# Optimization experiments

Hardware: AMD Instinct MI355X
Metric: run time of the kernel (lower is better)

The kernel has to match this reference:

```python
import jax, jax.numpy as jnp
import numpy as np

Q, S, D = 8192, 30, 512
THRESH = 30


def setup_inputs() -> dict:
    key = jax.random.key(0)
    ks = jax.random.split(key, 8)
    return {
        "query_encode": jax.random.normal(ks[0], (Q, D), jnp.float32),
        "support_encode": jax.random.normal(ks[1], (S, D), jnp.float32),
        # binary CTR-style labels in {0,1}
        "support_y": jnp.round(jax.random.uniform(ks[2], (1, S), jnp.float32)),
        "support_predict": jax.random.normal(ks[3], (S,), jnp.float32),
        "query_predict": jax.random.normal(ks[4], (Q,), jnp.float32),
        "fc1_w": jax.random.normal(ks[5], (D,), jnp.float32) / np.sqrt(D),
        "fc1_b": jnp.zeros((), jnp.float32),
        # AdjustLayer params: scale init 6, bias init 0, shape [THRESH, 1]
        "adjust_scale": jnp.full((THRESH, 1), 6.0, jnp.float32),
        "adjust_bias": jnp.zeros((THRESH, 1), jnp.float32),
        "num_samples": S,
    }


def reference(query_encode, support_encode, support_y, support_predict,
              query_predict, fc1_w, fc1_b, adjust_scale, adjust_bias,
              num_samples):
    # Pairwise L1 distance: [Q, S, D]
    distance = jnp.abs(query_encode[:, None, :] - support_encode[None, :, :])
    # Linear scorer over feature dim -> [Q, S]
    similar_score = jnp.einsum("qsd,d->qs", distance, fc1_w) + fc1_b
    attn = jax.nn.softmax(similar_score, axis=1)  # softmax over support dim
    # Residual of support labels vs predictor output: [1, S]
    delta_y = support_y - jax.nn.sigmoid(support_predict)[None, :]
    delta_y_hat = jnp.sum(delta_y * attn, axis=1)  # [Q]
    # AdjustLayer: indexed scale/bias (index is a static int here)
    scale = jnp.abs(adjust_scale[num_samples - 1, 0])
    bias = adjust_bias[num_samples - 1, 0]
    prediction = delta_y_hat * scale + bias + query_predict  # [Q]
    # Mean L2 distance to support set: [Q]
    mean_l2 = jnp.mean(jnp.sqrt(jnp.sum(distance ** 2, axis=-1)), axis=-1)
    return prediction, mean_l2
```

## Files before the change

kernel.cpp:

```cpp
#include <hip/hip_runtime.h>
#include <math.h>


#define QN 8192
#define SN 30
#define DN 512
#define QPB 16
#define BLK 512
#define RS 516

__global__ __launch_bounds__(BLK, 2)
void resus_one(const float* __restrict__ query,
               const float* __restrict__ support,
               const float* __restrict__ support_y,
               const float* __restrict__ support_pr,
               const float* __restrict__ query_pr,
               const float* __restrict__ fc1_w,
               const float* __restrict__ adj_scale,
               const float* __restrict__ adj_bias,
               const int*   __restrict__ num_samples,
               float* __restrict__ out)
{
    __shared__ float s_lds[SN * RS];

    const int tid = threadIdx.x;

    {
        const float4* sg = reinterpret_cast<const float4*>(support);
        for (int i = tid; i < SN * (DN / 4); i += BLK) {
            const int row = i >> 7;
            const int c4  = i & 127;
            *reinterpret_cast<float4*>(s_lds + row * RS + 4 * c4) = sg[i];
        }
    }
    __syncthreads();

    const int lane = tid & 63;
    const int wv   = tid >> 6;
    const int h    = lane >> 5;
    const int s    = lane & 31;
    const int srow_i = (s < SN) ? s : (SN - 1);

    const int q0 = blockIdx.x * QPB + wv * 2;
    const int q1 = q0 + 1;

    const float* srow = s_lds + srow_i * RS + h * 256;
    const float* qr0  = query + (size_t)q0 * DN + h * 256;
    const float* qr1  = query + (size_t)q1 * DN + h * 256;
    const float* wr   = fc1_w + h * 256;

    float sc0 = 0.f, sq0 = 0.f, sc1 = 0.f, sq1 = 0.f;

#define ACC4(QV, SV, WV, SC, SQ) { \
    float d0_ = (QV).x - (SV).x; SC = fmaf((WV).x, fabsf(d0_), SC); SQ = fmaf(d0_, d0_, SQ); \
    float d1_ = (QV).y - (SV).y; SC = fmaf((WV).y, fabsf(d1_), SC); SQ = fmaf(d1_, d1_, SQ); \
    float d2_ = (QV).z - (SV).z; SC = fmaf((WV).z, fabsf(d2_), SC); SQ = fmaf(d2_, d2_, SQ); \
    float d3_ = (QV).w - (SV).w; SC = fmaf((WV).w, fabsf(d3_), SC); SQ = fmaf(d3_, d3_, SQ); }

#pragma unroll 4
    for (int j = 0; j < 32; ++j) {
        const float4 sa = *reinterpret_cast<const float4*>(srow + 8 * j);
        const float4 sb = *reinterpret_cast<const float4*>(srow + 8 * j + 4);
        const float4 wa = *reinterpret_cast<const float4*>(wr + 8 * j);
        const float4 wb = *reinterpret_cast<const float4*>(wr + 8 * j + 4);
        const float4 a0 = *reinterpret_cast<const float4*>(qr0 + 8 * j);
        const float4 b0 = *reinterpret_cast<const float4*>(qr0 + 8 * j + 4);
        const float4 a1 = *reinterpret_cast<const float4*>(qr1 + 8 * j);
        const float4 b1 = *reinterpret_cast<const float4*>(qr1 + 8 * j + 4);
        ACC4(a0, sa, wa, sc0, sq0)
        ACC4(b0, sb, wb, sc0, sq0)
        ACC4(a1, sa, wa, sc1, sq1)
        ACC4(b1, sb, wb, sc1, sq1)
    }
#undef ACC4

    sc0 += __shfl_xor(sc0, 32);
    sq0 += __shfl_xor(sq0, 32);
    sc1 += __shfl_xor(sc1, 32);
    sq1 += __shfl_xor(sq1, 32);

    const bool valid = (s < SN);
    float scv = h ? sc1 : sc0;
    float ssv = h ? sq1 : sq0;
    const int q = h ? q1 : q0;

    float dy = 0.f;
    if (valid)
        dy = support_y[s] - 1.0f / (1.0f + expf(-support_pr[s]));
    if (!valid) { scv = -1e30f; ssv = 0.f; }

    float m = scv;
#pragma unroll
    for (int off = 16; off >= 1; off >>= 1)
        m = fmaxf(m, __shfl_xor(m, off));

    float e   = valid ? expf(scv - m) : 0.f;
    float den = e;
    float num = dy * e;
    float l2  = valid ? sqrtf(ssv) : 0.f;
#pragma unroll
    for (int off = 16; off >= 1; off >>= 1) {
        den += __shfl_xor(den, off);
        num += __shfl_xor(num, off);
        l2  += __shfl_xor(l2, off);
    }

    if (s == 0) {
        const int ns = num_samples[0];
        const float scale = fabsf(adj_scale[ns - 1]);
        const float bias  = adj_bias[ns - 1];
        out[q]      = num / den * scale + bias + query_pr[q];
        out[QN + q] = l2 * (1.0f / (float)SN);
    }
}

extern "C" void kernel_launch(void* const* d_in, const int* in_sizes, int n_in,
                              void* d_out, int out_size, void* d_ws, size_t ws_size,
                              hipStream_t stream)
{
    const float* query      = (const float*)d_in[0];
    const float* support    = (const float*)d_in[1];
    const float* support_y  = (const float*)d_in[2];
    const float* support_pr = (const float*)d_in[3];
    const float* query_pr   = (const float*)d_in[4];
    const float* fc1_w      = (const float*)d_in[5];
    const float* adj_scale  = (const float*)d_in[7];
    const float* adj_bias   = (const float*)d_in[8];
    const int*   num_s      = (const int*)d_in[9];
    float* out = (float*)d_out;

    dim3 grid(QN / QPB);
    hipLaunchKernelGGL(resus_one, grid, dim3(BLK), 0, stream,
                       query, support, support_y, support_pr, query_pr,
                       fc1_w, adj_scale, adj_bias, num_s, out);
}
```

Before: 105.2 us.

## Process four queries per wave with prefetched query loads and odd LDS stride

```diff
diff --git a/kernel.cpp b/kernel.cpp
--- a/kernel.cpp
+++ b/kernel.cpp
@@ -5,9 +5,11 @@
 #define QN 8192
 #define SN 30
 #define DN 512
-#define QPB 16
 #define BLK 512
-#define RS 516
+#define WPB 8
+#define QPW 4
+#define QPB (WPB * QPW)
+#define RS 515
 
 __global__ __launch_bounds__(BLK, 2)
 void resus_one(const float* __restrict__ query,
@@ -23,95 +25,128 @@
 {
     __shared__ float s_lds[SN * RS];
 
-    const int tid = threadIdx.x;
-
-    {
-        const float4* sg = reinterpret_cast<const float4*>(support);
-        for (int i = tid; i < SN * (DN / 4); i += BLK) {
-            const int row = i >> 7;
-            const int c4  = i & 127;
-            *reinterpret_cast<float4*>(s_lds + row * RS + 4 * c4) = sg[i];
-        }
-    }
-    __syncthreads();
-
+    const int tid  = threadIdx.x;
     const int lane = tid & 63;
     const int wv   = tid >> 6;
     const int h    = lane >> 5;
     const int s    = lane & 31;
     const int srow_i = (s < SN) ? s : (SN - 1);
 
-    const int q0 = blockIdx.x * QPB + wv * 2;
-    const int q1 = q0 + 1;
+    const int qbase = blockIdx.x * QPB + wv * QPW;
 
+    const float* qr0 = query + (size_t)(qbase + 0) * DN + h * 256;
+    const float* qr1 = query + (size_t)(qbase + 1) * DN + h * 256;
+    const float* qr2 = query + (size_t)(qbase + 2) * DN + h * 256;
+    const float* qr3 = query + (size_t)(qbase + 3) * DN + h * 256;
+    const float* wr  = fc1_w + h * 256;
     const float* srow = s_lds + srow_i * RS + h * 256;
-    const float* qr0  = query + (size_t)q0 * DN + h * 256;
-    const float* qr1  = query + (size_t)q1 * DN + h * 256;
-    const float* wr   = fc1_w + h * 256;
+
+    float4 c0a = *reinterpret_cast<const float4*>(qr0);
+    float4 c0b = *reinterpret_cast<const float4*>(qr0 + 4);
+    float4 c1a = *reinterpret_cast<const float4*>(qr1);
+    float4 c1b = *reinterpret_cast<const float4*>(qr1 + 4);
+    float4 c2a = *reinterpret_cast<const float4*>(qr2);
+    float4 c2b = *reinterpret_cast<const float4*>(qr2 + 4);
+    float4 c3a = *reinterpret_cast<const float4*>(qr3);
+    float4 c3b = *reinterpret_cast<const float4*>(qr3 + 4);
+    float4 cwa = *reinterpret_cast<const float4*>(wr);
+    float4 cwb = *reinterpret_cast<const float4*>(wr + 4);
+
+    {
+        const float4* sg = reinterpret_cast<const float4*>(support);
+        for (int i = tid; i < SN * (DN / 4); i += BLK) {
+            const float4 v = sg[i];
+            float* d = s_lds + (i >> 7) * RS + 4 * (i & 127);
+            d[0] = v.x; d[1] = v.y; d[2] = v.z; d[3] = v.w;
+        }
+    }
+    __syncthreads();
 
     float sc0 = 0.f, sq0 = 0.f, sc1 = 0.f, sq1 = 0.f;
+    float sc2 = 0.f, sq2 = 0.f, sc3 = 0.f, sq3 = 0.f;
 
-#define ACC4(QV, SV, WV, SC, SQ) { \
-    float d0_ = (QV).x - (SV).x; SC = fmaf((WV).x, fabsf(d0_), SC); SQ = fmaf(d0_, d0_, SQ); \
-    float d1_ = (QV).y - (SV).y; SC = fmaf((WV).y, fabsf(d1_), SC); SQ = fmaf(d1_, d1_, SQ); \
-    float d2_ = (QV).z - (SV).z; SC = fmaf((WV).z, fabsf(d2_), SC); SQ = fmaf(d2_, d2_, SQ); \
-    float d3_ = (QV).w - (SV).w; SC = fmaf((WV).w, fabsf(d3_), SC); SQ = fmaf(d3_, d3_, SQ); }
+#define ACC8(CA, CB, SC, SQ) { float d_; \
+    d_ = (CA).x - s0; SC = fmaf(cwa.x, fabsf(d_), SC); SQ = fmaf(d_, d_, SQ); \
+    d_ = (CA).y - s1; SC = fmaf(cwa.y, fabsf(d_), SC); SQ = fmaf(d_, d_, SQ); \
+    d_ = (CA).z - s2; SC = fmaf(cwa.z, fabsf(d_), SC); SQ = fmaf(d_, d_, SQ); \
+    d_ = (CA).w - s3; SC = fmaf(cwa.w, fabsf(d_), SC); SQ = fmaf(d_, d_, SQ); \
+    d_ = (CB).x - s4; SC = fmaf(cwb.x, fabsf(d_), SC); SQ = fmaf(d_, d_, SQ); \
+    d_ = (CB).y - s5; SC = fmaf(cwb.y, fabsf(d_), SC); SQ = fmaf(d_, d_, SQ); \
+    d_ = (CB).z - s6; SC = fmaf(cwb.z, fabsf(d_), SC); SQ = fmaf(d_, d_, SQ); \
+    d_ = (CB).w - s7; SC = fmaf(cwb.w, fabsf(d_), SC); SQ = fmaf(d_, d_, SQ); }
 
 #pragma unroll 4
     for (int j = 0; j < 32; ++j) {
-        const float4 sa = *reinterpret_cast<const float4*>(srow + 8 * j);
-        const float4 sb = *reinterpret_cast<const float4*>(srow + 8 * j + 4);
-        const float4 wa = *reinterpret_cast<const float4*>(wr + 8 * j);
-        const float4 wb = *reinterpret_cast<const float4*>(wr + 8 * j + 4);
-        const float4 a0 = *reinterpret_cast<const float4*>(qr0 + 8 * j);
-        const float4 b0 = *reinterpret_cast<const float4*>(qr0 + 8 * j + 4);
-        const float4 a1 = *reinterpret_cast<const float4*>(qr1 + 8 * j);
-        const float4 b1 = *reinterpret_cast<const float4*>(qr1 + 8 * j + 4);
-        ACC4(a0, sa, wa, sc0, sq0)
-        ACC4(b0, sb, wb, sc0, sq0)
-        ACC4(a1, sa, wa, sc1, sq1)
-        ACC4(b1, sb, wb, sc1, sq1)
+        const int jn = (j + 1) & 31;
+        float4 n0a = *reinterpret_cast<const float4*>(qr0 + 8 * jn);
+        float4 n0b = *reinterpret_cast<const float4*>(qr0 + 8 * jn + 4);
+        float4 n1a = *reinterpret_cast<const float4*>(qr1 + 8 * jn);
+        float4 n1b = *reinterpret_cast<const float4*>(qr1 + 8 * jn + 4);
+        float4 n2a = *reinterpret_cast<const float4*>(qr2 + 8 * jn);
+        float4 n2b = *reinterpret_cast<const float4*>(qr2 + 8 * jn + 4);
+        float4 n3a = *reinterpret_cast<const float4*>(qr3 + 8 * jn);
+        float4 n3b = *reinterpret_cast<const float4*>(qr3 + 8 * jn + 4);
+        float4 nwa = *reinterpret_cast<const float4*>(wr + 8 * jn);
+        float4 nwb = *reinterpret_cast<const float4*>(wr + 8 * jn + 4);
+
+        const float* sp = srow + 8 * j;
+        const float s0 = sp[0], s1 = sp[1], s2 = sp[2], s3 = sp[3];
+        const float s4 = sp[4], s5 = sp[5], s6 = sp[6], s7 = sp[7];
+
+        ACC8(c0a, c0b, sc0, sq0)
+        ACC8(c1a, c1b, sc1, sq1)
+        ACC8(c2a, c2b, sc2, sq2)
+        ACC8(c3a, c3b, sc3, sq3)
+
+        c0a = n0a; c0b = n0b; c1a = n1a; c1b = n1b;
+        c2a = n2a; c2b = n2b; c3a = n3a; c3b = n3b;
+        cwa = nwa; cwb = nwb;
     }
-#undef ACC4
+#undef ACC8
 
-    sc0 += __shfl_xor(sc0, 32);
-    sq0 += __shfl_xor(sq0, 32);
-    sc1 += __shfl_xor(sc1, 32);
-    sq1 += __shfl_xor(sq1, 32);
+    sc0 += __shfl_xor(sc0, 32); sq0 += __shfl_xor(sq0, 32);
+    sc1 += __shfl_xor(sc1, 32); sq1 += __shfl_xor(sq1, 32);
+    sc2 += __shfl_xor(sc2, 32); sq2 += __shfl_xor(sq2, 32);
+    sc3 += __shfl_xor(sc3, 32); sq3 += __shfl_xor(sq3, 32);
 
     const bool valid = (s < SN);
-    float scv = h ? sc1 : sc0;
-    float ssv = h ? sq1 : sq0;
-    const int q = h ? q1 : q0;
-
     float dy = 0.f;
     if (valid)
         dy = support_y[s] - 1.0f / (1.0f + expf(-support_pr[s]));
-    if (!valid) { scv = -1e30f; ssv = 0.f; }
 
-    float m = scv;
-#pragma unroll
-    for (int off = 16; off >= 1; off >>= 1)
-        m = fmaxf(m, __shfl_xor(m, off));
+    const int ns = num_samples[0];
+    const float ascale = fabsf(adj_scale[ns - 1]);
+    const float abias  = adj_bias[ns - 1];
 
-    float e   = valid ? expf(scv - m) : 0.f;
-    float den = e;
-    float num = dy * e;
-    float l2  = valid ? sqrtf(ssv) : 0.f;
-#pragma unroll
-    for (int off = 16; off >= 1; off >>= 1) {
-        den += __shfl_xor(den, off);
-        num += __shfl_xor(num, off);
-        l2  += __shfl_xor(l2, off);
-    }
+    float scA = h ? sc2 : sc0;  float sqA = h ? sq2 : sq0;
+    float scB = h ? sc3 : sc1;  float sqB = h ? sq3 : sq1;
+    const int qA = qbase + 2 * h;
+    const int qB = qA + 1;
 
-    if (s == 0) {
-        const int ns = num_samples[0];
-        const float scale = fabsf(adj_scale[ns - 1]);
-        const float bias  = adj_bias[ns - 1];
-        out[q]      = num / den * scale + bias + query_pr[q];
-        out[QN + q] = l2 * (1.0f / (float)SN);
-    }
+#define FINISH(SCV, SQV, QI) { \
+    float scv = (SCV), ssv = (SQV); \
+    if (!valid) { scv = -1e30f; ssv = 0.f; } \
+    float m_ = scv; \
+    _Pragma("unroll") \
+    for (int off = 16; off >= 1; off >>= 1) m_ = fmaxf(m_, __shfl_xor(m_, off)); \
+    float e_   = valid ? expf(scv - m_) : 0.f; \
+    float den_ = e_; \
+    float num_ = dy * e_; \
+    float l2_  = valid ? sqrtf(ssv) : 0.f; \
+    _Pragma("unroll") \
+    for (int off = 16; off >= 1; off >>= 1) { \
+        den_ += __shfl_xor(den_, off); \
+        num_ += __shfl_xor(num_, off); \
+        l2_  += __shfl_xor(l2_,  off); \
+    } \
+    if (s == 0) { \
+        out[(QI)]      = num_ / den_ * ascale + abias + query_pr[(QI)]; \
+        out[QN + (QI)] = l2_ * (1.0f / (float)SN); \
+    } }
+
+    FINISH(scA, sqA, qA)
+    FINISH(scB, sqB, qB)
+#undef FINISH
 }
 
 extern "C" void kernel_launch(void* const* d_in, const int* in_sizes, int n_in,
```

Measured after the change: 104.5 us. No clear change (-0.7%).

## Keep query slices in registers and stream support rows through LDS with atomic partials

Applied to the files above, without the earlier changes.

```diff
diff --git a/kernel.cpp b/kernel.cpp
--- a/kernel.cpp
+++ b/kernel.cpp
@@ -5,9 +5,10 @@
 #define QN 8192
 #define SN 30
 #define DN 512
-#define QPB 16
-#define BLK 512
-#define RS 516
+#define BLK 256
+#define QT 16
+#define SROW 572
+#define SCHUNK 15
 
 __global__ __launch_bounds__(BLK, 2)
 void resus_one(const float* __restrict__ query,
@@ -21,96 +22,125 @@
                const int*   __restrict__ num_samples,
                float* __restrict__ out)
 {
-    __shared__ float s_lds[SN * RS];
+    __shared__ float  sp[SCHUNK * SROW];
+    __shared__ float2 part[QT * SN];
 
-    const int tid = threadIdx.x;
+    const int tid  = threadIdx.x;
+    const int ql   = tid & 15;
+    const int dseg = tid >> 4;
+    const int q    = blockIdx.x * QT + ql;
 
     {
-        const float4* sg = reinterpret_cast<const float4*>(support);
-        for (int i = tid; i < SN * (DN / 4); i += BLK) {
-            const int row = i >> 7;
-            const int c4  = i & 127;
-            *reinterpret_cast<float4*>(s_lds + row * RS + 4 * c4) = sg[i];
+        float* pf = reinterpret_cast<float*>(part);
+        for (int i = tid; i < QT * SN * 2; i += BLK) pf[i] = 0.0f;
+    }
+
+    const float* qp = query + (size_t)q * DN + dseg * 32;
+    const float4 q0 = *reinterpret_cast<const float4*>(qp +  0);
+    const float4 q1 = *reinterpret_cast<const float4*>(qp +  4);
+    const float4 q2 = *reinterpret_cast<const float4*>(qp +  8);
+    const float4 q3 = *reinterpret_cast<const float4*>(qp + 12);
+    const float4 q4 = *reinterpret_cast<const float4*>(qp + 16);
+    const float4 q5 = *reinterpret_cast<const float4*>(qp + 20);
+    const float4 q6 = *reinterpret_cast<const float4*>(qp + 24);
+    const float4 q7 = *reinterpret_cast<const float4*>(qp + 28);
+    const float* wp = fc1_w + dseg * 32;
+    const float4 w0 = *reinterpret_cast<const float4*>(wp +  0);
+    const float4 w1 = *reinterpret_cast<const float4*>(wp +  4);
+    const float4 w2 = *reinterpret_cast<const float4*>(wp +  8);
+    const float4 w3 = *reinterpret_cast<const float4*>(wp + 12);
+    const float4 w4 = *reinterpret_cast<const float4*>(wp + 16);
+    const float4 w5 = *reinterpret_cast<const float4*>(wp + 20);
+    const float4 w6 = *reinterpret_cast<const float4*>(wp + 24);
+    const float4 w7 = *reinterpret_cast<const float4*>(wp + 28);
+
+    const int sbase = dseg * 36;
+
+#define ACC4(QV, WV, SV) { float d_; \
+    d_ = (QV).x - (SV).x; sc = fmaf((WV).x, fabsf(d_), sc); sq = fmaf(d_, d_, sq); \
+    d_ = (QV).y - (SV).y; sc = fmaf((WV).y, fabsf(d_), sc); sq = fmaf(d_, d_, sq); \
+    d_ = (QV).z - (SV).z; sc = fmaf((WV).z, fabsf(d_), sc); sq = fmaf(d_, d_, sq); \
+    d_ = (QV).w - (SV).w; sc = fmaf((WV).w, fabsf(d_), sc); sq = fmaf(d_, d_, sq); }
+
+    for (int pass = 0; pass < 2; ++pass) {
+        __syncthreads();
+
+        const float4* sg = reinterpret_cast<const float4*>(
+            support + (size_t)pass * SCHUNK * DN);
+        for (int i = tid; i < SCHUNK * 128; i += BLK) {
+            const int row = i >> 7, c4 = i & 127;
+            *reinterpret_cast<float4*>(
+                sp + row * SROW + 36 * (c4 >> 3) + 4 * (c4 & 7)) = sg[i];
+        }
+        __syncthreads();
+
+#pragma unroll 3
+        for (int sl = 0; sl < SCHUNK; ++sl) {
+            const float* sr = sp + sl * SROW + sbase;
+            const float4 s0 = *reinterpret_cast<const float4*>(sr +  0);
+            const float4 s1 = *reinterpret_cast<const float4*>(sr +  4);
+            const float4 s2 = *reinterpret_cast<const float4*>(sr +  8);
+            const float4 s3 = *reinterpret_cast<const float4*>(sr + 12);
+            const float4 s4 = *reinterpret_cast<const float4*>(sr + 16);
+            const float4 s5 = *reinterpret_cast<const float4*>(sr + 20);
+            const float4 s6 = *reinterpret_cast<const float4*>(sr + 24);
+            const float4 s7 = *reinterpret_cast<const float4*>(sr + 28);
+
+            float sc = 0.0f, sq = 0.0f;
+            ACC4(q0, w0, s0) ACC4(q1, w1, s1)
+            ACC4(q2, w2, s2) ACC4(q3, w3, s3)
+            ACC4(q4, w4, s4) ACC4(q5, w5, s5)
+            ACC4(q6, w6, s6) ACC4(q7, w7, s7)
+
+            const int sglob = pass * SCHUNK + sl;
+            atomicAdd(&part[ql * SN + sglob].x, sc);
+            atomicAdd(&part[ql * SN + sglob].y, sq);
         }
     }
+#undef ACC4
     __syncthreads();
 
-    const int lane = tid & 63;
-    const int wv   = tid >> 6;
-    const int h    = lane >> 5;
-    const int s    = lane & 31;
-    const int srow_i = (s < SN) ? s : (SN - 1);
+    const int grp   = tid >> 5;
+    const int s32   = tid & 31;
+    const bool valid = (s32 < SN);
 
-    const int q0 = blockIdx.x * QPB + wv * 2;
-    const int q1 = q0 + 1;
+    float dy = 0.0f;
+    if (valid)
+        dy = support_y[s32] - 1.0f / (1.0f + expf(-support_pr[s32]));
 
-    const float* srow = s_lds + srow_i * RS + h * 256;
-    const float* qr0  = query + (size_t)q0 * DN + h * 256;
-    const float* qr1  = query + (size_t)q1 * DN + h * 256;
-    const float* wr   = fc1_w + h * 256;
+    const int ns = num_samples[0];
+    const float ascale = fabsf(adj_scale[ns - 1]);
+    const float abias  = adj_bias[ns - 1];
 
-    float sc0 = 0.f, sq0 = 0.f, sc1 = 0.f, sq1 = 0.f;
+#pragma unroll
+    for (int it = 0; it < 2; ++it) {
+        const int qloc = grp + 8 * it;
+        const int qg   = blockIdx.x * QT + qloc;
+        const float2 pr = part[qloc * SN + (valid ? s32 : 0)];
 
-#define ACC4(QV, SV, WV, SC, SQ) { \
-    float d0_ = (QV).x - (SV).x; SC = fmaf((WV).x, fabsf(d0_), SC); SQ = fmaf(d0_, d0_, SQ); \
-    float d1_ = (QV).y - (SV).y; SC = fmaf((WV).y, fabsf(d1_), SC); SQ = fmaf(d1_, d1_, SQ); \
-    float d2_ = (QV).z - (SV).z; SC = fmaf((WV).z, fabsf(d2_), SC); SQ = fmaf(d2_, d2_, SQ); \
-    float d3_ = (QV).w - (SV).w; SC = fmaf((WV).w, fabsf(d3_), SC); SQ = fmaf(d3_, d3_, SQ); }
+        float scv = valid ? pr.x : -1e30f;
+        float ssv = valid ? pr.y : 0.0f;
 
-#pragma unroll 4
-    for (int j = 0; j < 32; ++j) {
-        const float4 sa = *reinterpret_cast<const float4*>(srow + 8 * j);
-        const float4 sb = *reinterpret_cast<const float4*>(srow + 8 * j + 4);
-        const float4 wa = *reinterpret_cast<const float4*>(wr + 8 * j);
-        const float4 wb = *reinterpret_cast<const float4*>(wr + 8 * j + 4);
-        const float4 a0 = *reinterpret_cast<const float4*>(qr0 + 8 * j);
-        const float4 b0 = *reinterpret_cast<const float4*>(qr0 + 8 * j + 4);
-        const float4 a1 = *reinterpret_cast<const float4*>(qr1 + 8 * j);
-        const float4 b1 = *reinterpret_cast<const float4*>(qr1 + 8 * j + 4);
-        ACC4(a0, sa, wa, sc0, sq0)
-        ACC4(b0, sb, wb, sc0, sq0)
-        ACC4(a1, sa, wa, sc1, sq1)
-        ACC4(b1, sb, wb, sc1, sq1)
-    }
-#undef ACC4
+        float m = scv;
+#pragma unroll
+        for (int off = 16; off >= 1; off >>= 1)
+            m = fmaxf(m, __shfl_xor(m, off));
 
-    sc0 += __shfl_xor(sc0, 32);
-    sq0 += __shfl_xor(sq0, 32);
-    sc1 += __shfl_xor(sc1, 32);
-    sq1 += __shfl_xor(sq1, 32);
+        float e   = valid ? expf(scv - m) : 0.0f;
+        float den = e;
+        float num = dy * e;
+        float l2  = valid ? sqrtf(ssv) : 0.0f;
+#pragma unroll
+        for (int off = 16; off >= 1; off >>= 1) {
+            den += __shfl_xor(den, off);
+            num += __shfl_xor(num, off);
+            l2  += __shfl_xor(l2,  off);
+        }
 
-    const bool valid = (s < SN);
-    float scv = h ? sc1 : sc0;
-    float ssv = h ? sq1 : sq0;
-    const int q = h ? q1 : q0;
-
-    float dy = 0.f;
-    if (valid)
-        dy = support_y[s] - 1.0f / (1.0f + expf(-support_pr[s]));
-    if (!valid) { scv = -1e30f; ssv = 0.f; }
-
-    float m = scv;
-#pragma unroll
-    for (int off = 16; off >= 1; off >>= 1)
-        m = fmaxf(m, __shfl_xor(m, off));
-
-    float e   = valid ? expf(scv - m) : 0.f;
-    float den = e;
-    float num = dy * e;
-    float l2  = valid ? sqrtf(ssv) : 0.f;
-#pragma unroll
-    for (int off = 16; off >= 1; off >>= 1) {
-        den += __shfl_xor(den, off);
-        num += __shfl_xor(num, off);
-        l2  += __shfl_xor(l2, off);
-    }
-
-    if (s == 0) {
-        const int ns = num_samples[0];
-        const float scale = fabsf(adj_scale[ns - 1]);
-        const float bias  = adj_bias[ns - 1];
-        out[q]      = num / den * scale + bias + query_pr[q];
-        out[QN + q] = l2 * (1.0f / (float)SN);
+        if (s32 == 0) {
+            out[qg]      = num / den * ascale + abias + query_pr[qg];
+            out[QN + qg] = l2 * (1.0f / (float)SN);
+        }
     }
 }
 
@@ -129,7 +159,7 @@
     const int*   num_s      = (const int*)d_in[9];
     float* out = (float*)d_out;
 
-    dim3 grid(QN / QPB);
+    dim3 grid(QN / QT);
     hipLaunchKernelGGL(resus_one, grid, dim3(BLK), 0, stream,
                        query, support, support_y, support_pr, query_pr,
                        fc1_w, adj_scale, adj_bias, num_s, out);
```

Measured after the change: 129.3 us. 22.8% more time.
